# Kernel optimization log

Measured on AMD Instinct MI355X. Metric: run time of the kernel, lower is better.

Reference implementation:

```python
import jax, jax.numpy as jnp
import numpy as np

Q_DIM = 512
K_DIM = 512
V_DIM = 512
H_DIM = 256
B, Q, K = 4, 512, 512


def setup_inputs() -> dict:
    key = jax.random.key(0)
    ks = jax.random.split(key, 7)
    q = jax.random.normal(ks[0], (B, Q, Q_DIM), dtype=jnp.float32)
    k = jax.random.normal(ks[1], (B, K, K_DIM), dtype=jnp.float32)
    v = jax.random.normal(ks[2], (B, K, V_DIM), dtype=jnp.float32)
    S = jax.random.randint(ks[3], (B,), 1, K + 1, dtype=jnp.int64)
    # learned params (nn.Linear stores weight of shape (out, in); y = x @ W.T)
    Wq = jax.random.normal(ks[4], (H_DIM, Q_DIM), dtype=jnp.float32) / np.sqrt(Q_DIM)
    Wk = jax.random.normal(ks[5], (H_DIM, K_DIM), dtype=jnp.float32) / np.sqrt(K_DIM)
    w = jax.random.normal(ks[6], (H_DIM,), dtype=jnp.float32) / np.sqrt(H_DIM)
    return {"q": q, "k": k, "v": v, "S": S, "Wq": Wq, "Wk": Wk, "w": w}


def reference(q, k, v, S, Wq, Wk, w):
    # Additive (Bahdanau) attention scores.
    pq = jnp.einsum('bqd,hd->bqh', q, Wq)            # (B, Q, H)
    pk = jnp.einsum('bkd,hd->bkh', k, Wk)            # (B, K, H)
    t = jnp.tanh(pq[:, :, None, :] + pk[:, None, :, :])  # (B, Q, K, H)
    scores = jnp.einsum('bqkh,h->bqk', t, w)         # (B, Q, K)
    # mask keys with index >= S[b] to -inf
    kv_idx = jnp.arange(scores.shape[-1])            # (K,)
    mask = kv_idx[None, None, :] >= S[:, None, None] # (B, 1, K) -> broadcast
    scores = jnp.where(mask, -jnp.inf, scores)
    return scores
```

## Files before the change

kernel.cpp:

```cpp
#include <hip/hip_runtime.h>
#include <hip/hip_bf16.h>
#include <math.h>

#define QDIM 512
#define HDIM 256
#define QQ 512
#define KKE 512

#define TWO_LOG2E 2.8853900817779268f
#define MASK_VAL -1.0e30f

typedef __attribute__((ext_vector_type(8))) short bf16x8;
typedef __attribute__((ext_vector_type(4))) float f32x4;

__device__ __forceinline__ unsigned int pk2(float x, float y) {
  __hip_bfloat162 h = __float22bfloat162_rn(make_float2(x, y));
  unsigned int u;
  __builtin_memcpy(&u, &h, 4);
  return u;
}

__global__ __launch_bounds__(512) void proj_kernel(
    const float* __restrict__ qin, const float* __restrict__ kin,
    const float* __restrict__ Wq, const float* __restrict__ Wk,
    const float* __restrict__ wvec,
    float* __restrict__ EqT, unsigned short* __restrict__ EkT,
    float* __restrict__ wsum_out) {
  __shared__ __align__(16) unsigned short As[32 * 72];
  __shared__ __align__(16) unsigned short Bs[64 * 72];

  const int tid = threadIdx.x;
  const int lane = tid & 63;
  const int wv = __builtin_amdgcn_readfirstlane(tid >> 6);
  const int quad = lane >> 4;
  const int l16 = lane & 15;

  const int m0 = blockIdx.x * 32;
  const int h0 = blockIdx.y * 64;
  const bool isk = (blockIdx.z != 0);
  const float* A = isk ? kin : qin;
  const float* W = isk ? Wk : Wq;

  const int srow = tid >> 4;
  const int sg = (tid & 15) * 4;

  const float* arow_g = &A[(size_t)(m0 + srow) * QDIM + sg];
  const float* brow0_g = &W[(size_t)(h0 + srow) * QDIM + sg];
  const float* brow1_g = &W[(size_t)(h0 + srow + 32) * QDIM + sg];
  unsigned short* adst = &As[srow * 72 + sg];
  unsigned short* bdst0 = &Bs[srow * 72 + sg];
  unsigned short* bdst1 = &Bs[(srow + 32) * 72 + sg];

  const unsigned short* afrag = &As[((wv & 1) * 16 + l16) * 72 + quad * 8];
  const unsigned short* bfrag = &Bs[((wv >> 1) * 16 + l16) * 72 + quad * 8];

  f32x4 acc = (f32x4){0.f, 0.f, 0.f, 0.f};

  for (int kc = 0; kc < QDIM; kc += 64) {
    __syncthreads();
    {
      float4 va = *(const float4*)(arow_g + kc);
      float4 vb0 = *(const float4*)(brow0_g + kc);
      float4 vb1 = *(const float4*)(brow1_g + kc);
      *(uint2*)adst = make_uint2(pk2(va.x, va.y), pk2(va.z, va.w));
      *(uint2*)bdst0 = make_uint2(pk2(vb0.x, vb0.y), pk2(vb0.z, vb0.w));
      *(uint2*)bdst1 = make_uint2(pk2(vb1.x, vb1.y), pk2(vb1.z, vb1.w));
    }
    __syncthreads();
    bf16x8 a0 = *(const bf16x8*)afrag;
    bf16x8 a1 = *(const bf16x8*)(afrag + 32);
    bf16x8 b0 = *(const bf16x8*)bfrag;
    bf16x8 b1 = *(const bf16x8*)(bfrag + 32);
    acc = __builtin_amdgcn_mfma_f32_16x16x32_bf16(a0, b0, acc, 0, 0, 0);
    acc = __builtin_amdgcn_mfma_f32_16x16x32_bf16(a1, b1, acc, 0, 0, 0);
  }

  const int b = m0 >> 9;
  const int hrow = h0 + (wv >> 1) * 16 + l16;
  const int mcol = (m0 & 511) + (wv & 1) * 16 + quad * 4;
  float e0 = __builtin_amdgcn_exp2f(acc[0] * TWO_LOG2E);
  float e1 = __builtin_amdgcn_exp2f(acc[1] * TWO_LOG2E);
  float e2 = __builtin_amdgcn_exp2f(acc[2] * TWO_LOG2E);
  float e3 = __builtin_amdgcn_exp2f(acc[3] * TWO_LOG2E);
  if (!isk) {
    *(float4*)(EqT + ((size_t)b * HDIM + hrow) * 512 + mcol) =
        make_float4(e0, e1, e2, e3);
    if (m0 == 0 && h0 == 0 && tid < 64) {
      float s = wvec[tid] + wvec[tid + 64] + wvec[tid + 128] + wvec[tid + 192];
#pragma unroll
      for (int off = 32; off; off >>= 1) s += __shfl_down(s, off);
      if (tid == 0) wsum_out[0] = s;
    }
  } else {
    *(uint2*)(EkT + ((size_t)b * HDIM + hrow) * 512 + mcol) =
        make_uint2(pk2(e0, e1), pk2(e2, e3));
  }
}

__global__ __launch_bounds__(256) void score_kernel(
    const float* __restrict__ EqT, const unsigned short* __restrict__ EkT,
    const float* __restrict__ wvec, const float* __restrict__ wsump,
    const int* __restrict__ Sraw, float* __restrict__ out) {
  const int b = blockIdx.z;
  const int q0 = blockIdx.y * 8;
  const int k0 = blockIdx.x * 32;
  const int S = (Sraw[1] == 0) ? Sraw[2 * b] : Sraw[b];
  const int tid = threadIdx.x;
  const int wv = __builtin_amdgcn_readfirstlane(tid >> 6);
  const int L = tid & 63;
  const int q = L >> 3;
  const int k4 = (L & 7) * 4;
  float* orow = out + ((size_t)(b * QQ + q0 + q) * KKE + k0 + k4);

  if (k0 >= S) {
    if (wv == 0)
      *(float4*)orow = make_float4(MASK_VAL, MASK_VAL, MASK_VAL, MASK_VAL);
    return;
  }

  __shared__ float Eqs[256][8];
  __shared__ unsigned short Eks[256][32];
  __shared__ float Cmb[3][64][4];

  {
    const float* EqB = EqT + (size_t)b * (HDIM * QQ) + q0;
    const unsigned short* EkB = EkT + (size_t)b * (HDIM * KKE) + k0;
    const int hq = tid >> 1, cq = (tid & 1) * 4;
    *(float4*)&Eqs[hq][cq] = *(const float4*)&EqB[(size_t)hq * QQ + cq];
    *(float4*)&Eqs[hq + 128][cq] = *(const float4*)&EqB[(size_t)(hq + 128) * QQ + cq];
    const int hk = tid >> 2, ck = (tid & 3) * 8;
#pragma unroll
    for (int p = 0; p < 4; p++)
      *(uint4*)&Eks[hk + p * 64][ck] =
          *(const uint4*)&EkB[(size_t)(hk + p * 64) * KKE + ck];
  }
  __syncthreads();

  float a0 = 0.f, a1 = 0.f, a2 = 0.f, a3 = 0.f;
  const int hbase = wv * 64;
#pragma unroll 4
  for (int hh = 0; hh < 64; hh++) {
    const int h = hbase + hh;
    float wh = wvec[h];
    float eq = Eqs[h][q];
    uint2 u = *(const uint2*)&Eks[h][k4];
    float e0 = __uint_as_float(u.x << 16);
    float e1 = __uint_as_float(u.x & 0xffff0000u);
    float e2 = __uint_as_float(u.y << 16);
    float e3 = __uint_as_float(u.y & 0xffff0000u);
    a0 = fmaf(wh, __builtin_amdgcn_rcpf(fmaf(eq, e0, 1.f)), a0);
    a1 = fmaf(wh, __builtin_amdgcn_rcpf(fmaf(eq, e1, 1.f)), a1);
    a2 = fmaf(wh, __builtin_amdgcn_rcpf(fmaf(eq, e2, 1.f)), a2);
    a3 = fmaf(wh, __builtin_amdgcn_rcpf(fmaf(eq, e3, 1.f)), a3);
  }

  if (wv > 0) {
    Cmb[wv - 1][L][0] = a0; Cmb[wv - 1][L][1] = a1;
    Cmb[wv - 1][L][2] = a2; Cmb[wv - 1][L][3] = a3;
  }
  __syncthreads();
  if (wv == 0) {
    a0 += Cmb[0][L][0] + Cmb[1][L][0] + Cmb[2][L][0];
    a1 += Cmb[0][L][1] + Cmb[1][L][1] + Cmb[2][L][1];
    a2 += Cmb[0][L][2] + Cmb[1][L][2] + Cmb[2][L][2];
    a3 += Cmb[0][L][3] + Cmb[1][L][3] + Cmb[2][L][3];
    const float wsum = wsump[0];
    const int kb = k0 + k4;
    float4 r;
    r.x = (kb + 0 < S) ? (wsum - 2.f * a0) : MASK_VAL;
    r.y = (kb + 1 < S) ? (wsum - 2.f * a1) : MASK_VAL;
    r.z = (kb + 2 < S) ? (wsum - 2.f * a2) : MASK_VAL;
    r.w = (kb + 3 < S) ? (wsum - 2.f * a3) : MASK_VAL;
    *(float4*)orow = r;
  }
}

extern "C" void kernel_launch(void* const* d_in, const int* in_sizes, int n_in,
                              void* d_out, int out_size, void* d_ws, size_t ws_size,
                              hipStream_t stream) {
  const float* q  = (const float*)d_in[0];
  const float* k  = (const float*)d_in[1];
  const int*   S  = (const int*)d_in[3];
  const float* Wq = (const float*)d_in[4];
  const float* Wk = (const float*)d_in[5];
  const float* w  = (const float*)d_in[6];
  float* out = (float*)d_out;

  float* wsf = (float*)d_ws;
  float* EqT = wsf;
  unsigned short* EkT = (unsigned short*)(wsf + 524288);
  float* wsum = wsf + 524288 + 262144;

  proj_kernel<<<dim3(64, 4, 2), 512, 0, stream>>>(q, k, Wq, Wk, w, EqT, EkT, wsum);
  score_kernel<<<dim3(16, 64, 4), 256, 0, stream>>>(EqT, EkT, w, wsum, S, out);
}
```

Baseline: 113.1 us.

## Enlarge score tile, pair K tiles for load balance, prefetch projection loads

The score kernel now handles 16 queries by 8 keys per thread-group tile. Each block processes two key tiles (i and 15-i) to even out work under the length mask, and caches w in shared memory. The projection kernel register-prefetches the next K chunk before the MFMA step to overlap global loads. The larger tile raises register and LDS use, and it reloads the Eq tile for each key tile.

```diff
diff --git a/kernel.cpp b/kernel.cpp
--- a/kernel.cpp
+++ b/kernel.cpp
@@ -56,15 +56,19 @@
 
   f32x4 acc = (f32x4){0.f, 0.f, 0.f, 0.f};
 
+  float4 pa = *(const float4*)arow_g;
+  float4 pb0 = *(const float4*)brow0_g;
+  float4 pb1 = *(const float4*)brow1_g;
+
   for (int kc = 0; kc < QDIM; kc += 64) {
     __syncthreads();
-    {
-      float4 va = *(const float4*)(arow_g + kc);
-      float4 vb0 = *(const float4*)(brow0_g + kc);
-      float4 vb1 = *(const float4*)(brow1_g + kc);
-      *(uint2*)adst = make_uint2(pk2(va.x, va.y), pk2(va.z, va.w));
-      *(uint2*)bdst0 = make_uint2(pk2(vb0.x, vb0.y), pk2(vb0.z, vb0.w));
-      *(uint2*)bdst1 = make_uint2(pk2(vb1.x, vb1.y), pk2(vb1.z, vb1.w));
+    *(uint2*)adst = make_uint2(pk2(pa.x, pa.y), pk2(pa.z, pa.w));
+    *(uint2*)bdst0 = make_uint2(pk2(pb0.x, pb0.y), pk2(pb0.z, pb0.w));
+    *(uint2*)bdst1 = make_uint2(pk2(pb1.x, pb1.y), pk2(pb1.z, pb1.w));
+    if (kc + 64 < QDIM) {
+      pa = *(const float4*)(arow_g + kc + 64);
+      pb0 = *(const float4*)(brow0_g + kc + 64);
+      pb1 = *(const float4*)(brow1_g + kc + 64);
     }
     __syncthreads();
     bf16x8 a0 = *(const bf16x8*)afrag;
@@ -102,76 +106,111 @@
     const float* __restrict__ wvec, const float* __restrict__ wsump,
     const int* __restrict__ Sraw, float* __restrict__ out) {
   const int b = blockIdx.z;
-  const int q0 = blockIdx.y * 8;
-  const int k0 = blockIdx.x * 32;
+  const int q0 = blockIdx.y * 16;
+  const int i = blockIdx.x;
   const int S = (Sraw[1] == 0) ? Sraw[2 * b] : Sraw[b];
   const int tid = threadIdx.x;
   const int wv = __builtin_amdgcn_readfirstlane(tid >> 6);
   const int L = tid & 63;
-  const int q = L >> 3;
-  const int k4 = (L & 7) * 4;
-  float* orow = out + ((size_t)(b * QQ + q0 + q) * KKE + k0 + k4);
-
-  if (k0 >= S) {
-    if (wv == 0)
-      *(float4*)orow = make_float4(MASK_VAL, MASK_VAL, MASK_VAL, MASK_VAL);
-    return;
-  }
-
-  __shared__ float Eqs[256][8];
+  const int q = L >> 2;
+  const int k8 = (L & 3) * 8;
+
+  __shared__ float wl[HDIM];
+  __shared__ float Eqs[256][16];
   __shared__ unsigned short Eks[256][32];
-  __shared__ float Cmb[3][64][4];
-
-  {
-    const float* EqB = EqT + (size_t)b * (HDIM * QQ) + q0;
-    const unsigned short* EkB = EkT + (size_t)b * (HDIM * KKE) + k0;
-    const int hq = tid >> 1, cq = (tid & 1) * 4;
-    *(float4*)&Eqs[hq][cq] = *(const float4*)&EqB[(size_t)hq * QQ + cq];
-    *(float4*)&Eqs[hq + 128][cq] = *(const float4*)&EqB[(size_t)(hq + 128) * QQ + cq];
-    const int hk = tid >> 2, ck = (tid & 3) * 8;
-#pragma unroll
-    for (int p = 0; p < 4; p++)
-      *(uint4*)&Eks[hk + p * 64][ck] =
-          *(const uint4*)&EkB[(size_t)(hk + p * 64) * KKE + ck];
-  }
-  __syncthreads();
-
-  float a0 = 0.f, a1 = 0.f, a2 = 0.f, a3 = 0.f;
-  const int hbase = wv * 64;
+  __shared__ float Cmb[3][64][8];
+  wl[tid] = wvec[tid];
+
+  const float wsum = wsump[0];
+  const float* EqB = EqT + (size_t)b * (HDIM * QQ) + q0;
+  const unsigned short* EkB0 = EkT + (size_t)b * (HDIM * KKE);
+
+#pragma unroll
+  for (int t = 0; t < 2; ++t) {
+    const int kt = t ? (15 - i) : i;
+    const int k0 = kt * 32;
+    float* orow = out + ((size_t)(b * QQ + q0 + q) * KKE + k0 + k8);
+
+    if (k0 >= S) {
+      if (wv == 0) {
+        float4 m4 = make_float4(MASK_VAL, MASK_VAL, MASK_VAL, MASK_VAL);
+        *(float4*)&orow[0] = m4;
+        *(float4*)&orow[4] = m4;
+      }
+      continue;
+    }
+
+    __syncthreads();
+    {
+      const unsigned short* EkB = EkB0 + k0;
+      const int hr = tid >> 2;
+      const int cq = (tid & 3) * 4;
+      const int ce = (tid & 3) * 8;
+#pragma unroll
+      for (int p = 0; p < 4; p++) {
+        *(float4*)&Eqs[hr + p * 64][cq] =
+            *(const float4*)&EqB[(size_t)(hr + p * 64) * QQ + cq];
+        *(uint4*)&Eks[hr + p * 64][ce] =
+            *(const uint4*)&EkB[(size_t)(hr + p * 64) * KKE + ce];
+      }
+    }
+    __syncthreads();
+
+    float a0 = 0.f, a1 = 0.f, a2 = 0.f, a3 = 0.f;
+    float a4 = 0.f, a5 = 0.f, a6 = 0.f, a7 = 0.f;
+    const int hbase = wv * 64;
 #pragma unroll 4
-  for (int hh = 0; hh < 64; hh++) {
-    const int h = hbase + hh;
-    float wh = wvec[h];
-    float eq = Eqs[h][q];
-    uint2 u = *(const uint2*)&Eks[h][k4];
-    float e0 = __uint_as_float(u.x << 16);
-    float e1 = __uint_as_float(u.x & 0xffff0000u);
-    float e2 = __uint_as_float(u.y << 16);
-    float e3 = __uint_as_float(u.y & 0xffff0000u);
-    a0 = fmaf(wh, __builtin_amdgcn_rcpf(fmaf(eq, e0, 1.f)), a0);
-    a1 = fmaf(wh, __builtin_amdgcn_rcpf(fmaf(eq, e1, 1.f)), a1);
-    a2 = fmaf(wh, __builtin_amdgcn_rcpf(fmaf(eq, e2, 1.f)), a2);
-    a3 = fmaf(wh, __builtin_amdgcn_rcpf(fmaf(eq, e3, 1.f)), a3);
-  }
-
-  if (wv > 0) {
-    Cmb[wv - 1][L][0] = a0; Cmb[wv - 1][L][1] = a1;
-    Cmb[wv - 1][L][2] = a2; Cmb[wv - 1][L][3] = a3;
-  }
-  __syncthreads();
-  if (wv == 0) {
-    a0 += Cmb[0][L][0] + Cmb[1][L][0] + Cmb[2][L][0];
-    a1 += Cmb[0][L][1] + Cmb[1][L][1] + Cmb[2][L][1];
-    a2 += Cmb[0][L][2] + Cmb[1][L][2] + Cmb[2][L][2];
-    a3 += Cmb[0][L][3] + Cmb[1][L][3] + Cmb[2][L][3];
-    const float wsum = wsump[0];
-    const int kb = k0 + k4;
-    float4 r;
-    r.x = (kb + 0 < S) ? (wsum - 2.f * a0) : MASK_VAL;
-    r.y = (kb + 1 < S) ? (wsum - 2.f * a1) : MASK_VAL;
-    r.z = (kb + 2 < S) ? (wsum - 2.f * a2) : MASK_VAL;
-    r.w = (kb + 3 < S) ? (wsum - 2.f * a3) : MASK_VAL;
-    *(float4*)orow = r;
+    for (int hh = 0; hh < 64; hh++) {
+      const int h = hbase + hh;
+      float wh = wl[h];
+      float eq = Eqs[h][q];
+      uint4 u = *(const uint4*)&Eks[h][k8];
+      float e0 = __uint_as_float(u.x << 16);
+      float e1 = __uint_as_float(u.x & 0xffff0000u);
+      float e2 = __uint_as_float(u.y << 16);
+      float e3 = __uint_as_float(u.y & 0xffff0000u);
+      float e4 = __uint_as_float(u.z << 16);
+      float e5 = __uint_as_float(u.z & 0xffff0000u);
+      float e6 = __uint_as_float(u.w << 16);
+      float e7 = __uint_as_float(u.w & 0xffff0000u);
+      a0 = fmaf(wh, __builtin_amdgcn_rcpf(fmaf(eq, e0, 1.f)), a0);
+      a1 = fmaf(wh, __builtin_amdgcn_rcpf(fmaf(eq, e1, 1.f)), a1);
+      a2 = fmaf(wh, __builtin_amdgcn_rcpf(fmaf(eq, e2, 1.f)), a2);
+      a3 = fmaf(wh, __builtin_amdgcn_rcpf(fmaf(eq, e3, 1.f)), a3);
+      a4 = fmaf(wh, __builtin_amdgcn_rcpf(fmaf(eq, e4, 1.f)), a4);
+      a5 = fmaf(wh, __builtin_amdgcn_rcpf(fmaf(eq, e5, 1.f)), a5);
+      a6 = fmaf(wh, __builtin_amdgcn_rcpf(fmaf(eq, e6, 1.f)), a6);
+      a7 = fmaf(wh, __builtin_amdgcn_rcpf(fmaf(eq, e7, 1.f)), a7);
+    }
+
+    if (wv > 0) {
+      Cmb[wv - 1][L][0] = a0; Cmb[wv - 1][L][1] = a1;
+      Cmb[wv - 1][L][2] = a2; Cmb[wv - 1][L][3] = a3;
+      Cmb[wv - 1][L][4] = a4; Cmb[wv - 1][L][5] = a5;
+      Cmb[wv - 1][L][6] = a6; Cmb[wv - 1][L][7] = a7;
+    }
+    __syncthreads();
+    if (wv == 0) {
+#pragma unroll
+      for (int c = 0; c < 3; c++) {
+        a0 += Cmb[c][L][0]; a1 += Cmb[c][L][1];
+        a2 += Cmb[c][L][2]; a3 += Cmb[c][L][3];
+        a4 += Cmb[c][L][4]; a5 += Cmb[c][L][5];
+        a6 += Cmb[c][L][6]; a7 += Cmb[c][L][7];
+      }
+      const int kb = k0 + k8;
+      float4 r0, r1;
+      r0.x = (kb + 0 < S) ? (wsum - 2.f * a0) : MASK_VAL;
+      r0.y = (kb + 1 < S) ? (wsum - 2.f * a1) : MASK_VAL;
+      r0.z = (kb + 2 < S) ? (wsum - 2.f * a2) : MASK_VAL;
+      r0.w = (kb + 3 < S) ? (wsum - 2.f * a3) : MASK_VAL;
+      r1.x = (kb + 4 < S) ? (wsum - 2.f * a4) : MASK_VAL;
+      r1.y = (kb + 5 < S) ? (wsum - 2.f * a5) : MASK_VAL;
+      r1.z = (kb + 6 < S) ? (wsum - 2.f * a6) : MASK_VAL;
+      r1.w = (kb + 7 < S) ? (wsum - 2.f * a7) : MASK_VAL;
+      *(float4*)&orow[0] = r0;
+      *(float4*)&orow[4] = r1;
+    }
   }
 }
 
@@ -192,5 +231,5 @@
   float* wsum = wsf + 524288 + 262144;
 
   proj_kernel<<<dim3(64, 4, 2), 512, 0, stream>>>(q, k, Wq, Wk, w, EqT, EkT, wsum);
-  score_kernel<<<dim3(16, 64, 4), 256, 0, stream>>>(EqT, EkT, w, wsum, S, out);
-}
+  score_kernel<<<dim3(8, 32, 4), 256, 0, stream>>>(EqT, EkT, w, wsum, S, out);
+}
```

New measurement: 97.82 us. 13.5% less time.

## Rebalance score kernel work across blocks and prefetch projection loads

Applied to the files above, without the earlier changes.

The score kernel now gives each block 16 query rows and two key tiles, paired as i and 15-i, so the masked work is spread evenly across blocks. Each wave owns whole outputs and loops over all 256 hidden units, which removes the cross-wave LDS reduction. Eq and w are staged in LDS once per block. The projection kernel also prefetches the next chunk's global loads into registers before the MFMA step. The cost is fewer blocks, a longer serial loop per thread, and an added occupancy hint.

```diff
diff --git a/kernel.cpp b/kernel.cpp
--- a/kernel.cpp
+++ b/kernel.cpp
@@ -56,15 +56,19 @@
 
   f32x4 acc = (f32x4){0.f, 0.f, 0.f, 0.f};
 
+  float4 pa = *(const float4*)arow_g;
+  float4 pb0 = *(const float4*)brow0_g;
+  float4 pb1 = *(const float4*)brow1_g;
+
   for (int kc = 0; kc < QDIM; kc += 64) {
     __syncthreads();
-    {
-      float4 va = *(const float4*)(arow_g + kc);
-      float4 vb0 = *(const float4*)(brow0_g + kc);
-      float4 vb1 = *(const float4*)(brow1_g + kc);
-      *(uint2*)adst = make_uint2(pk2(va.x, va.y), pk2(va.z, va.w));
-      *(uint2*)bdst0 = make_uint2(pk2(vb0.x, vb0.y), pk2(vb0.z, vb0.w));
-      *(uint2*)bdst1 = make_uint2(pk2(vb1.x, vb1.y), pk2(vb1.z, vb1.w));
+    *(uint2*)adst = make_uint2(pk2(pa.x, pa.y), pk2(pa.z, pa.w));
+    *(uint2*)bdst0 = make_uint2(pk2(pb0.x, pb0.y), pk2(pb0.z, pb0.w));
+    *(uint2*)bdst1 = make_uint2(pk2(pb1.x, pb1.y), pk2(pb1.z, pb1.w));
+    if (kc + 64 < QDIM) {
+      pa = *(const float4*)(arow_g + kc + 64);
+      pb0 = *(const float4*)(brow0_g + kc + 64);
+      pb1 = *(const float4*)(brow1_g + kc + 64);
     }
     __syncthreads();
     bf16x8 a0 = *(const bf16x8*)afrag;
@@ -97,81 +101,80 @@
   }
 }
 
-__global__ __launch_bounds__(256) void score_kernel(
+__global__ __launch_bounds__(256, 4) void score_kernel(
     const float* __restrict__ EqT, const unsigned short* __restrict__ EkT,
     const float* __restrict__ wvec, const float* __restrict__ wsump,
     const int* __restrict__ Sraw, float* __restrict__ out) {
   const int b = blockIdx.z;
-  const int q0 = blockIdx.y * 8;
-  const int k0 = blockIdx.x * 32;
+  const int q0 = blockIdx.y * 16;
+  const int i = blockIdx.x;
   const int S = (Sraw[1] == 0) ? Sraw[2 * b] : Sraw[b];
   const int tid = threadIdx.x;
   const int wv = __builtin_amdgcn_readfirstlane(tid >> 6);
   const int L = tid & 63;
-  const int q = L >> 3;
-  const int k4 = (L & 7) * 4;
-  float* orow = out + ((size_t)(b * QQ + q0 + q) * KKE + k0 + k4);
+  const int q = 4 * wv + (L >> 4);
+  const int k2 = (L & 15) * 2;
 
-  if (k0 >= S) {
-    if (wv == 0)
-      *(float4*)orow = make_float4(MASK_VAL, MASK_VAL, MASK_VAL, MASK_VAL);
-    return;
-  }
-
-  __shared__ float Eqs[256][8];
-  __shared__ unsigned short Eks[256][32];
-  __shared__ float Cmb[3][64][4];
+  __shared__ float wl[HDIM];
+  __shared__ float Eqs[HDIM][16];
+  __shared__ unsigned short Eks[HDIM][32];
 
   {
-    const float* EqB = EqT + (size_t)b * (HDIM * QQ) + q0;
-    const unsigned short* EkB = EkT + (size_t)b * (HDIM * KKE) + k0;
-    const int hq = tid >> 1, cq = (tid & 1) * 4;
-    *(float4*)&Eqs[hq][cq] = *(const float4*)&EqB[(size_t)hq * QQ + cq];
-    *(float4*)&Eqs[hq + 128][cq] = *(const float4*)&EqB[(size_t)(hq + 128) * QQ + cq];
-    const int hk = tid >> 2, ck = (tid & 3) * 8;
+    const float* src = EqT + ((size_t)b * HDIM + tid) * QQ + q0;
+    float4 v0 = *(const float4*)(src + 0);
+    float4 v1 = *(const float4*)(src + 4);
+    float4 v2 = *(const float4*)(src + 8);
+    float4 v3 = *(const float4*)(src + 12);
+    *(float4*)&Eqs[tid][0] = v0;
+    *(float4*)&Eqs[tid][4] = v1;
+    *(float4*)&Eqs[tid][8] = v2;
+    *(float4*)&Eqs[tid][12] = v3;
+    wl[tid] = wvec[tid];
+  }
+  const float wsum = wsump[0];
+  const unsigned short* EkB = EkT + (size_t)b * (HDIM * KKE);
+
 #pragma unroll
-    for (int p = 0; p < 4; p++)
-      *(uint4*)&Eks[hk + p * 64][ck] =
-          *(const uint4*)&EkB[(size_t)(hk + p * 64) * KKE + ck];
-  }
-  __syncthreads();
+  for (int t = 0; t < 2; ++t) {
+    const int k0 = (t ? (15 - i) : i) * 32;
+    float* op = out + ((size_t)(b * QQ + q0 + q) * KKE + k0 + k2);
 
-  float a0 = 0.f, a1 = 0.f, a2 = 0.f, a3 = 0.f;
-  const int hbase = wv * 64;
-#pragma unroll 4
-  for (int hh = 0; hh < 64; hh++) {
-    const int h = hbase + hh;
-    float wh = wvec[h];
-    float eq = Eqs[h][q];
-    uint2 u = *(const uint2*)&Eks[h][k4];
-    float e0 = __uint_as_float(u.x << 16);
-    float e1 = __uint_as_float(u.x & 0xffff0000u);
-    float e2 = __uint_as_float(u.y << 16);
-    float e3 = __uint_as_float(u.y & 0xffff0000u);
-    a0 = fmaf(wh, __builtin_amdgcn_rcpf(fmaf(eq, e0, 1.f)), a0);
-    a1 = fmaf(wh, __builtin_amdgcn_rcpf(fmaf(eq, e1, 1.f)), a1);
-    a2 = fmaf(wh, __builtin_amdgcn_rcpf(fmaf(eq, e2, 1.f)), a2);
-    a3 = fmaf(wh, __builtin_amdgcn_rcpf(fmaf(eq, e3, 1.f)), a3);
-  }
+    if (k0 >= S) {
+      *(float2*)op = make_float2(MASK_VAL, MASK_VAL);
+      continue;
+    }
 
-  if (wv > 0) {
-    Cmb[wv - 1][L][0] = a0; Cmb[wv - 1][L][1] = a1;
-    Cmb[wv - 1][L][2] = a2; Cmb[wv - 1][L][3] = a3;
-  }
-  __syncthreads();
-  if (wv == 0) {
-    a0 += Cmb[0][L][0] + Cmb[1][L][0] + Cmb[2][L][0];
-    a1 += Cmb[0][L][1] + Cmb[1][L][1] + Cmb[2][L][1];
-    a2 += Cmb[0][L][2] + Cmb[1][L][2] + Cmb[2][L][2];
-    a3 += Cmb[0][L][3] + Cmb[1][L][3] + Cmb[2][L][3];
-    const float wsum = wsump[0];
-    const int kb = k0 + k4;
-    float4 r;
+    __syncthreads();
+    {
+      const unsigned short* sk = EkB + (size_t)tid * KKE + k0;
+      uint4 u0 = *(const uint4*)(sk + 0);
+      uint4 u1 = *(const uint4*)(sk + 8);
+      uint4 u2 = *(const uint4*)(sk + 16);
+      uint4 u3 = *(const uint4*)(sk + 24);
+      *(uint4*)&Eks[tid][0] = u0;
+      *(uint4*)&Eks[tid][8] = u1;
+      *(uint4*)&Eks[tid][16] = u2;
+      *(uint4*)&Eks[tid][24] = u3;
+    }
+    __syncthreads();
+
+    float a0 = 0.f, a1 = 0.f;
+#pragma unroll 8
+    for (int h = 0; h < HDIM; ++h) {
+      float wh = wl[h];
+      float eq = Eqs[h][q];
+      unsigned int u = *(const unsigned int*)&Eks[h][k2];
+      float e0 = __uint_as_float(u << 16);
+      float e1 = __uint_as_float(u & 0xffff0000u);
+      a0 = fmaf(wh, __builtin_amdgcn_rcpf(fmaf(eq, e0, 1.f)), a0);
+      a1 = fmaf(wh, __builtin_amdgcn_rcpf(fmaf(eq, e1, 1.f)), a1);
+    }
+
+    const int kb = k0 + k2;
+    float2 r;
     r.x = (kb + 0 < S) ? (wsum - 2.f * a0) : MASK_VAL;
     r.y = (kb + 1 < S) ? (wsum - 2.f * a1) : MASK_VAL;
-    r.z = (kb + 2 < S) ? (wsum - 2.f * a2) : MASK_VAL;
-    r.w = (kb + 3 < S) ? (wsum - 2.f * a3) : MASK_VAL;
-    *(float4*)orow = r;
+    *(float2*)op = r;
   }
 }
 
@@ -192,5 +195,5 @@
   float* wsum = wsf + 524288 + 262144;
 
   proj_kernel<<<dim3(64, 4, 2), 512, 0, stream>>>(q, k, Wq, Wk, w, EqT, EkT, wsum);
-  score_kernel<<<dim3(16, 64, 4), 256, 0, stream>>>(EqT, EkT, w, wsum, S, out);
+  score_kernel<<<dim3(8, 32, 4), 256, 0, stream>>>(EqT, EkT, w, wsum, S, out);
 }
```

Measured after the change: 99.71 us. -11.8%, faster.
